# Kernel tuning notes

Hardware: AMD Instinct MI355X
Metric: run time of the kernel (lower is better)

The kernel has to match this reference:

```python
import jax, jax.numpy as jnp
from jax import lax
import numpy as np

B, C, H, W = 2, 64, 192, 192

def conv2d(x, w, pad):
    return lax.conv_general_dilated(x, w, (1, 1), [(pad, pad), (pad, pad)],
                                    dimension_numbers=('NCHW', 'OIHW', 'NCHW'))

def bilinear_sample(x, py, px):
    # x: [B,C,H,W]; py, px: [B,H,W] absolute fractional coords; zero padding outside.
    Bb, Cc, Hh, Ww = x.shape
    y0 = jnp.floor(py); x0 = jnp.floor(px)
    wy1 = py - y0; wx1 = px - x0
    xf = x.reshape(Bb, Cc, Hh * Ww)
    def gather(yi, xi):
        valid = (yi >= 0) & (yi < Hh) & (xi >= 0) & (xi < Ww)
        yc = jnp.clip(yi, 0, Hh - 1).astype(jnp.int32)
        xc = jnp.clip(xi, 0, Ww - 1).astype(jnp.int32)
        idx = (yc * Ww + xc).reshape(Bb, 1, Hh * Ww)
        v = jnp.take_along_axis(xf, idx, axis=2).reshape(Bb, Cc, Hh, Ww)
        return v * valid[:, None].astype(x.dtype)
    return (gather(y0, x0) * ((1 - wy1) * (1 - wx1))[:, None]
            + gather(y0, x0 + 1) * ((1 - wy1) * wx1)[:, None]
            + gather(y0 + 1, x0) * (wy1 * (1 - wx1))[:, None]
            + gather(y0 + 1, x0 + 1) * (wy1 * wx1)[:, None])

def deform_conv(x, w_off, b_off, w_mod, b_mod, w_reg, k):
    # torchvision deform_conv2d semantics with modulation (mask), stride=1, dilation=1.
    pad = k // 2
    offset = conv2d(x, w_off, pad) + b_off[None, :, None, None]   # [B,2*k*k,H,W] (y,x) interleaved
    mask = 2.0 * jax.nn.sigmoid(conv2d(x, w_mod, pad) + b_mod[None, :, None, None])  # [B,k*k,H,W]
    Bb, Cc, Hh, Ww = x.shape
    gy = jnp.arange(Hh, dtype=x.dtype)[None, :, None]
    gx = jnp.arange(Ww, dtype=x.dtype)[None, None, :]
    out = jnp.zeros((Bb, w_reg.shape[0], Hh, Ww), x.dtype)
    for i in range(k):          # fixed structural loop over kernel taps
        for j in range(k):
            t = i * k + j
            py = gy - pad + i + offset[:, 2 * t]
            px = gx - pad + j + offset[:, 2 * t + 1]
            samp = bilinear_sample(x, py, px) * mask[:, t][:, None]  # [B,C,H,W]
            out = out + jnp.einsum('bchw,oc->bohw', samp, w_reg[:, :, i, j])
    return out

def _branch(x, w_pre, w_off, b_off, w_mod, b_mod, w_reg, k):
    h = jax.nn.relu(conv2d(x, w_pre, 0))  # BasicConv 1x1 + ReLU (no bias)
    return deform_conv(h, w_off, b_off, w_mod, b_mod, w_reg, k)

def _forward(x_max, x_mid, x_small,
             w_pre_max, w_off_max, b_off_max, w_mod_max, b_mod_max, w_reg_max,
             w_pre_mid, w_off_mid, b_off_mid, w_mod_mid, b_mod_mid, w_reg_mid,
             w_pre_small, w_off_small, b_off_small, w_mod_small, b_mod_small, w_reg_small,
             w1, w2):
    y = x_max + x_mid + x_small
    a = _branch(x_max, w_pre_max, w_off_max, b_off_max, w_mod_max, b_mod_max, w_reg_max, 7)
    m = _branch(x_mid, w_pre_mid, w_off_mid, b_off_mid, w_mod_mid, b_mod_mid, w_reg_mid, 5)
    s = _branch(x_small, w_pre_small, w_off_small, b_off_small, w_mod_small, b_mod_small, w_reg_small, 3)
    x = jnp.tanh(m) * a
    x = jax.nn.relu(conv2d(x, w1, 0))
    x = jnp.tanh(s) * x
    x = jax.nn.relu(conv2d(x, w2, 0))
    return x + y

def setup_inputs() -> dict:
    key = jax.random.key(0)
    ks = jax.random.split(key, 32)
    d = {}
    d['x_max'] = jax.random.normal(ks[0], (B, C, H, W), jnp.float32)
    d['x_mid'] = jax.random.normal(ks[1], (B, C, H, W), jnp.float32)
    d['x_small'] = jax.random.normal(ks[2], (B, C, H, W), jnp.float32)
    i = 3
    for name, k in (('max', 7), ('mid', 5), ('small', 3)):
        d[f'w_pre_{name}'] = jax.random.normal(ks[i], (C, C, 1, 1), jnp.float32) * 0.05; i += 1
        d[f'w_off_{name}'] = jax.random.normal(ks[i], (2 * k * k, C, k, k), jnp.float32) * 0.01; i += 1
        d[f'b_off_{name}'] = jax.random.normal(ks[i], (2 * k * k,), jnp.float32) * 0.01; i += 1
        d[f'w_mod_{name}'] = jax.random.normal(ks[i], (k * k, C, k, k), jnp.float32) * 0.01; i += 1
        d[f'b_mod_{name}'] = jax.random.normal(ks[i], (k * k,), jnp.float32) * 0.01; i += 1
        d[f'w_reg_{name}'] = jax.random.normal(ks[i], (C, C, k, k), jnp.float32) * 0.02; i += 1
    d['w1'] = jax.random.normal(ks[i], (C, C, 1, 1), jnp.float32) * 0.05; i += 1
    d['w2'] = jax.random.normal(ks[i], (C, C, 1, 1), jnp.float32) * 0.05
    return d

def reference(x_max, x_mid, x_small,
              w_pre_max, w_off_max, b_off_max, w_mod_max, b_mod_max, w_reg_max,
              w_pre_mid, w_off_mid, b_off_mid, w_mod_mid, b_mod_mid, w_reg_mid,
              w_pre_small, w_off_small, b_off_small, w_mod_small, b_mod_small, w_reg_small,
              w1, w2):
    return _forward(x_max, x_mid, x_small,
                    w_pre_max, w_off_max, b_off_max, w_mod_max, b_mod_max, w_reg_max,
                    w_pre_mid, w_off_mid, b_off_mid, w_mod_mid, b_mod_mid, w_reg_mid,
                    w_pre_small, w_off_small, b_off_small, w_mod_small, b_mod_small, w_reg_small,
                    w1, w2)
```

## Files before the change

### kernel.cpp

```cpp
#include <hip/hip_runtime.h>
#include <hip/hip_bf16.h>
#include <math.h>

#define BB   2
#define CC   64
#define HH   192
#define WW   192
#define HW   (HH*WW)
#define HALO 3
#define HP   (HH + 2*HALO)
#define WP   (WW + 2*HALO)
#define PLANE (HP*WP)

typedef __attribute__((ext_vector_type(8))) _Float16 f16x8;
typedef __attribute__((ext_vector_type(4))) _Float16 f16x4;
typedef __attribute__((ext_vector_type(8))) unsigned short u16x8;
typedef __attribute__((ext_vector_type(4))) float f32x4;

__device__ __forceinline__ float fast_tanh(float x) {
    float e = __expf(2.f * x);
    return 1.f - 2.f * __builtin_amdgcn_rcpf(e + 1.f);
}
__device__ __forceinline__ f16x8 bc16(u16x8 v) { return __builtin_bit_cast(f16x8, v); }

__global__ __launch_bounds__(256) void conv_pre_k(
    const float* __restrict__ X0, const float* __restrict__ X1,
    const float* __restrict__ X2,
    const float* __restrict__ W0, const float* __restrict__ W1,
    const float* __restrict__ W2,
    u16x8* __restrict__ hp8all)
{
    __shared__ float wl[64*32];
    int tid = threadIdx.x;
    int oh  = blockIdx.y;
    int z   = blockIdx.z;
    const float* X = (z == 0) ? X0 : ((z == 1) ? X1 : X2);
    const float* W = (z == 0) ? W0 : ((z == 1) ? W1 : W2);
    u16x8* hp8 = hp8all + (size_t)z * ((size_t)BB*8*PLANE);

    #pragma unroll
    for (int n = 0; n < 8; n++) {
        int idx = tid + n*256;
        int op  = idx >> 6, c = idx & 63;
        wl[c*32 + op] = W[(size_t)(oh*32 + op)*64 + c];
    }
    __syncthreads();

    int p  = blockIdx.x*256 + tid;
    int b  = p / HW;
    int pp = p - b*HW;
    size_t base = (size_t)b*CC*HW + pp;

    float acc[32];
    #pragma unroll
    for (int o = 0; o < 32; o++) acc[o] = 0.f;

    #pragma unroll 4
    for (int c = 0; c < 64; c++) {
        float xv = X[base + (size_t)c*HW];
        const float4* w4 = (const float4*)(wl + c*32);
        #pragma unroll
        for (int q = 0; q < 8; q++) {
            float4 w = w4[q];
            acc[4*q+0] = fmaf(w.x, xv, acc[4*q+0]);
            acc[4*q+1] = fmaf(w.y, xv, acc[4*q+1]);
            acc[4*q+2] = fmaf(w.z, xv, acc[4*q+2]);
            acc[4*q+3] = fmaf(w.w, xv, acc[4*q+3]);
        }
    }

    int y = pp / WW, x = pp - y*WW;
    #pragma unroll
    for (int gq = 0; gq < 4; gq++) {
        u16x8 v;
        #pragma unroll
        for (int c = 0; c < 8; c++)
            v[c] = __builtin_bit_cast(unsigned short,
                     (_Float16)fmaxf(acc[gq*8+c], 0.f));
        hp8[(size_t)(b*8 + oh*4 + gq)*PLANE + (size_t)(y+HALO)*WP + (x+HALO)] = v;
    }
}

template<int MODE>
__global__ __launch_bounds__(256) void conv1x1_k(
    const _Float16* __restrict__ Xv, const _Float16* __restrict__ Mv,
    const float* __restrict__ W,
    const float* __restrict__ Y0, const float* __restrict__ Y1,
    const float* __restrict__ Y2,
    void* __restrict__ outv)
{
    __shared__ float wl[64*32];
    int tid = threadIdx.x;
    int oh  = blockIdx.y;
    #pragma unroll
    for (int n = 0; n < 8; n++) {
        int idx = tid + n*256;
        int op  = idx >> 6, c = idx & 63;
        wl[c*32 + op] = W[(size_t)(oh*32 + op)*64 + c];
    }
    __syncthreads();

    int p  = blockIdx.x*256 + tid;
    int b  = p / HW;
    int pp = p - b*HW;
    size_t base = (size_t)b*CC*HW + pp;

    float acc[32];
    #pragma unroll
    for (int o = 0; o < 32; o++) acc[o] = 0.f;

    #pragma unroll 4
    for (int c = 0; c < 64; c++) {
        float xv = (float)Xv[base + (size_t)c*HW];
        xv *= fast_tanh((float)Mv[base + (size_t)c*HW]);
        const float4* w4 = (const float4*)(wl + c*32);
        #pragma unroll
        for (int q = 0; q < 8; q++) {
            float4 w = w4[q];
            acc[4*q+0] = fmaf(w.x, xv, acc[4*q+0]);
            acc[4*q+1] = fmaf(w.y, xv, acc[4*q+1]);
            acc[4*q+2] = fmaf(w.z, xv, acc[4*q+2]);
            acc[4*q+3] = fmaf(w.w, xv, acc[4*q+3]);
        }
    }

    if (MODE == 1) {
        _Float16* op = (_Float16*)outv + base + (size_t)(oh*32)*HW;
        #pragma unroll
        for (int o = 0; o < 32; o++)
            op[(size_t)o*HW] = (_Float16)fmaxf(acc[o], 0.f);
    } else {
        float* op = (float*)outv + base + (size_t)(oh*32)*HW;
        size_t gi = base + (size_t)(oh*32)*HW;
        #pragma unroll
        for (int o = 0; o < 32; o++) {
            float yv = Y0[gi + (size_t)o*HW] + Y1[gi + (size_t)o*HW] + Y2[gi + (size_t)o*HW];
            op[(size_t)o*HW] = fmaxf(acc[o], 0.f) + yv;
        }
    }
}

template<int K>
__device__ void bake_wtb_dev(const float* __restrict__ Wreg,
                             f16x8* __restrict__ wtb, int t, int tid)
{
    constexpr int KK = K*K;
    for (int e = tid; e < 512; e += 256) {
        int kk = e >> 8, rem = e & 255;
        int ot = rem >> 6, l = rem & 63;
        int lr = l & 15, lg = l >> 4;
        int o  = ot*16 + lr;
        f16x8 v;
        #pragma unroll
        for (int j = 0; j < 8; j++) {
            int c = kk*32 + lg*8 + j;
            v[j] = (_Float16)Wreg[((size_t)o*CC + c)*KK + t];
        }
        wtb[(size_t)t*512 + e] = v;
    }
}
template<int K>
__device__ void bake_wbg_dev(const float* __restrict__ Woff,
                             const float* __restrict__ Wmod,
                             f16x8* __restrict__ wbg, int pos, int tid)
{
    constexpr int KK  = K*K;
    constexpr int NTF = (3*KK + 15)/16;
    for (int idx = tid; idx < 2*NTF*64; idx += 256) {
        int kk  = idx / (NTF*64);
        int rem = idx - kk*(NTF*64);
        int nt  = rem >> 6;
        int l   = rem & 63;
        int lg  = l >> 4, lr = l & 15;
        int n   = nt*16 + lr;
        f16x8 v;
        #pragma unroll
        for (int j = 0; j < 8; j++) {
            int c = kk*32 + lg*8 + j;
            float w = 0.f;
            if (n < 2*KK)      w = Woff[((size_t)n*CC + c)*KK + pos];
            else if (n < 3*KK) w = Wmod[((size_t)(n - 2*KK)*CC + c)*KK + pos];
            v[j] = (_Float16)w;
        }
        wbg[(size_t)pos*(2*NTF*64) + idx] = v;
    }
}
__global__ __launch_bounds__(256) void bake_all_k(
    const float* wreg7, const float* woff7, const float* wmod7,
    const float* wreg5, const float* woff5, const float* wmod5,
    const float* wreg3, const float* woff3, const float* wmod3,
    f16x8* wtb7, f16x8* wbg7, f16x8* wtb5, f16x8* wbg5,
    f16x8* wtb3, f16x8* wbg3)
{
    int blk = blockIdx.x, tid = threadIdx.x;
    if (blk < 49) {
        bake_wtb_dev<7>(wreg7, wtb7, blk, tid);
        bake_wbg_dev<7>(woff7, wmod7, wbg7, blk, tid);
    } else if (blk < 74) {
        int p = blk - 49;
        bake_wtb_dev<5>(wreg5, wtb5, p, tid);
        bake_wbg_dev<5>(woff5, wmod5, wbg5, p, tid);
    } else {
        int p = blk - 74;
        bake_wtb_dev<3>(wreg3, wtb3, p, tid);
        bake_wbg_dev<3>(woff3, wmod3, wbg3, p, tid);
    }
}

template<int K, int MT, int NS>
__global__ __launch_bounds__(256) void offmod_mfma_k(
    const u16x8* __restrict__ hp8,
    const f16x8* __restrict__ wbg,
    const float* __restrict__ Boff, const float* __restrict__ Bmod,
    _Float16* __restrict__ om)
{
    constexpr int PAD  = K/2;
    constexpr int KK   = K*K;
    constexpr int NTF  = (3*KK + 15)/16;
    constexpr int NT   = NTF/NS;
    constexpr int PBB  = HW/(64*MT);
    constexpr int NBLK = BB*PBB*NS;
    constexpr int PELEM = 2*NT*64;

    __shared__ f16x8 wl[2][PELEM];

    int raw = blockIdx.x;
    int swz = (raw & 7)*(NBLK >> 3) + (raw >> 3);
    int ng  = swz % NS;
    int s   = swz / NS;
    int b   = s / PBB;
    int blk = s - b*PBB;

    int tid  = threadIdx.x;
    int wave = tid >> 6;
    int l    = tid & 63;
    int lg   = l >> 4, lr = l & 15;
    int pxw  = blk*(4*MT*16) + wave*(MT*16);
    int y    = pxw / WW, x0 = pxw - y*WW;

    f32x4 acc[MT][NT];
    #pragma unroll
    for (int mt = 0; mt < MT; mt++)
        #pragma unroll
        for (int nt = 0; nt < NT; nt++) acc[mt][nt] = (f32x4)0.f;

    const u16x8* hb = hp8 + (size_t)(b*8)*PLANE;

    auto stage = [&](int buf, int pos) {
        #pragma unroll
        for (int ii = 0; ii < (PELEM + 255)/256; ii++) {
            int idx = tid + ii*256;
            if (PELEM % 256 == 0 || idx < PELEM) {
                int kk  = idx / (NT*64);
                int rem = idx - kk*(NT*64);
                int nt  = rem >> 6;
                int ll  = rem & 63;
                wl[buf][idx] = wbg[(size_t)pos*(2*NTF*64)
                                   + (size_t)(kk*NTF + ng*NT + nt)*64 + ll];
            }
        }
    };

    stage(0, 0);
    __syncthreads();

    int buf = 0;
    for (int pos = 0; pos < KK; pos++) {
        if (pos + 1 < KK) stage(buf ^ 1, pos + 1);

        int i = pos / K, j = pos - (pos/K)*K;
        int rbase = (y + HALO - PAD + i)*WP + (x0 + HALO - PAD + j);

        #pragma unroll
        for (int kk = 0; kk < 2; kk++) {
            const f16x8* G = (const f16x8*)(hb + (size_t)(kk*4 + lg)*PLANE + rbase);
            f16x8 a[MT];
            #pragma unroll
            for (int mt = 0; mt < MT; mt++) a[mt] = G[mt*16 + lr];
            #pragma unroll
            for (int nt = 0; nt < NT; nt++) {
                f16x8 bf = wl[buf][(kk*NT + nt)*64 + l];
                #pragma unroll
                for (int mt = 0; mt < MT; mt++)
                    acc[mt][nt] = __builtin_amdgcn_mfma_f32_16x16x32_f16(
                        a[mt], bf, acc[mt][nt], 0, 0, 0);
            }
        }
        __syncthreads();
        buf ^= 1;
    }

    #pragma unroll
    for (int nt = 0; nt < NT; nt++) {
        int n = ng*NT*16 + nt*16 + lr;
        if (n < 3*KK) {
            bool is_mask = (n >= 2*KK);
            float bias = is_mask ? Bmod[n - 2*KK] : Boff[n];
            _Float16* dst0 = om + ((size_t)b*3*KK + n)*HW + pxw + lg*4;
            #pragma unroll
            for (int mt = 0; mt < MT; mt++) {
                f32x4 v = acc[mt][nt];
                float v0 = v[0] + bias, v1 = v[1] + bias, v2 = v[2] + bias, v3 = v[3] + bias;
                if (is_mask) {
                    v0 = 2.f * __builtin_amdgcn_rcpf(1.f + __expf(-v0));
                    v1 = 2.f * __builtin_amdgcn_rcpf(1.f + __expf(-v1));
                    v2 = 2.f * __builtin_amdgcn_rcpf(1.f + __expf(-v2));
                    v3 = 2.f * __builtin_amdgcn_rcpf(1.f + __expf(-v3));
                }
                f16x4 o;
                o[0] = (_Float16)v0; o[1] = (_Float16)v1;
                o[2] = (_Float16)v2; o[3] = (_Float16)v3;
                *reinterpret_cast<f16x4*>(dst0 + mt*16) = o;
            }
        }
    }
}

template<int K>
__global__ __launch_bounds__(256, 4) void deform_mfma_k(
    const u16x8* __restrict__ hp8,
    const _Float16* __restrict__ om,
    const f16x8* __restrict__ wtb,
    _Float16* __restrict__ out)
{
    constexpr int PAD = K/2;
    constexpr int KK  = K*K;
    constexpr int NSB = HW/16;
    constexpr int HWW = K + 2;
    constexpr int WWW = 16 + K + 2;
    constexpr int WELEMS = 8*HWW*WWW;
    constexpr int NPT = KK*16;
    constexpr int COORD_B = NPT*8 + NPT*4 + ((NPT*2 + 15)/16)*16;
    constexpr int RED_B   = 2*64*16*4;
    constexpr int UNION_B = (COORD_B > RED_B ? COORD_B : RED_B);

    __shared__ u16x8 win[8][HWW][WWW];
    __shared__ __align__(16) char ubuf[UNION_B];

    f16x4*          hco  = (f16x4*)ubuf;
    unsigned*       gofs = (unsigned*)(ubuf + NPT*8);
    unsigned short* wofs = (unsigned short*)(ubuf + NPT*8 + NPT*4);

    int raw = blockIdx.x;
    int swz = (raw & 7)*((BB*NSB) >> 3) + (raw >> 3);
    int b = swz / NSB, strip = swz - b*NSB;

    int tid  = threadIdx.x;
    int wave = tid >> 6;
    int l    = tid & 63;
    int lg   = l >> 4;
    int lr   = l & 15;
    int th   = wave & 1;
    int kkh  = wave >> 1;
    int pxbase = strip*16;
    int y    = pxbase / WW;
    int xs   = pxbase - y*WW;

    int wy0 = y  + HALO - PAD - 1;
    int wx0 = xs + HALO - PAD - 1;

    {
        const u16x8* hbb = hp8 + (size_t)(b*8)*PLANE;
        for (int idx = tid; idx < WELEMS; idx += 256) {
            int g  = idx / (HWW*WWW);
            int r2 = idx - g*(HWW*WWW);
            int r  = r2 / WWW;
            int c2 = r2 - r*WWW;
            int gy = min(max(wy0 + r, 0), HP-1);
            int gx = min(max(wx0 + c2, 0), WP-1);
            win[g][r][c2] = hbb[(size_t)g*PLANE + gy*WP + gx];
        }
    }
    {
        const _Float16* ob = om + (size_t)b*3*KK*HW + pxbase;
        for (int idx = tid; idx < NPT; idx += 256) {
            int pxl = idx & 15, t = idx >> 4;
            float offy = (float)ob[(size_t)(2*t  )*HW + pxl];
            float offx = (float)ob[(size_t)(2*t+1)*HW + pxl];
            float mk   = (float)ob[(size_t)(2*KK+t)*HW + pxl];
            int i = t / K, j = t - (t/K)*K;
            float py  = (float)(y - PAD + i) + offy;
            float pxf = (float)(xs + pxl - PAD + j) + offx;
            float fy = floorf(py), fx = floorf(pxf);
            float wy1 = py - fy, wx1 = pxf - fx;
            int iy0 = (int)fy, ix0 = (int)fx;
            int Y0 = min(max(iy0, -1), HH) + HALO;
            int X0 = min(max(ix0, -1), WW) + HALO;
            int ry = Y0 - wy0, rx = X0 - wx0;
            bool in = ((unsigned)ry <= (unsigned)(HWW-2)) &
                      ((unsigned)rx <= (unsigned)(WWW-2));
            f16x4 h;
            h[0] = (_Float16)((1.f-wy1)*(1.f-wx1)*mk);
            h[1] = (_Float16)((1.f-wy1)*wx1*mk);
            h[2] = (_Float16)(wy1*(1.f-wx1)*mk);
            h[3] = (_Float16)(wy1*wx1*mk);
            hco[idx]  = h;
            gofs[idx] = (unsigned)(Y0*WP + X0);
            wofs[idx] = (unsigned short)((ry*WWW + rx) | (in ? 0 : 0x8000));
        }
    }
    __syncthreads();

    int t0 = (KK*th)/2, t1 = (KK*(th+1))/2;

    f32x4 acc[4];
    #pragma unroll
    for (int ot = 0; ot < 4; ot++) acc[ot] = (f32x4)0.f;

    const u16x8* hb   = hp8 + (size_t)(b*8 + kkh*4 + lg)*PLANE;
    const u16x8* wing = &win[kkh*4 + lg][0][0];

    #pragma unroll 1
    for (int t = t0; t < t1; t++) {
        int idx = t*16 + lr;
        f16x4 h = hco[idx];
        unsigned short wf = wofs[idx];
        bool in = (wf & 0x8000) == 0;

        f16x8 c0, c1, c2, c3;
        if (__all(in)) {
            const u16x8* Wp = wing + wf;
            c0 = bc16(Wp[0]);   c1 = bc16(Wp[1]);
            c2 = bc16(Wp[WWW]); c3 = bc16(Wp[WWW+1]);
        } else {
            const u16x8* G = hb + gofs[idx];
            c0 = bc16(G[0]);  c1 = bc16(G[1]);
            c2 = bc16(G[WP]); c3 = bc16(G[WP+1]);
        }

        f16x8 s = c0*h[0] + c1*h[1] + c2*h[2] + c3*h[3];

        const f16x8* bp = wtb + (size_t)t*8*64 + l;
        #pragma unroll
        for (int ot = 0; ot < 4; ot++) {
            acc[ot] = __builtin_amdgcn_mfma_f32_16x16x32_f16(
                s, bp[(size_t)(kkh*4 + ot)*64], acc[ot], 0, 0, 0);
        }
    }

    __syncthreads();
    float* redf = (float*)ubuf;
    #define RIDX(tt, o, g)  (((tt)*64 + (o))*16 + (((g) ^ ((o) & 3)) * 4))
    if (kkh == 1) {
        #pragma unroll
        for (int ot = 0; ot < 4; ot++) {
            int o = ot*16 + lr;
            *reinterpret_cast<f32x4*>(&redf[RIDX(th, o, lg)]) = acc[ot];
        }
    }
    __syncthreads();
    if (kkh == 0) {
        #pragma unroll
        for (int ot = 0; ot < 4; ot++) {
            int o = ot*16 + lr;
            acc[ot] += *reinterpret_cast<const f32x4*>(&redf[RIDX(th, o, lg)]);
        }
    }
    __syncthreads();
    if (kkh == 0 && th == 1) {
        #pragma unroll
        for (int ot = 0; ot < 4; ot++) {
            int o = ot*16 + lr;
            *reinterpret_cast<f32x4*>(&redf[RIDX(0, o, lg)]) = acc[ot];
        }
    }
    __syncthreads();
    if (kkh == 0 && th == 0) {
        _Float16* ob = out + (size_t)b*CC*HW + pxbase + lg*4;
        #pragma unroll
        for (int ot = 0; ot < 4; ot++) {
            int o = ot*16 + lr;
            f32x4 rr = *reinterpret_cast<const f32x4*>(&redf[RIDX(0, o, lg)]);
            rr += acc[ot];
            f16x4 v;
            v[0] = (_Float16)rr[0]; v[1] = (_Float16)rr[1];
            v[2] = (_Float16)rr[2]; v[3] = (_Float16)rr[3];
            *reinterpret_cast<f16x4*>(ob + (size_t)o*HW) = v;
        }
    }
    #undef RIDX
}

extern "C" void kernel_launch(void* const* d_in, const int* in_sizes, int n_in,
                              void* d_out, int out_size, void* d_ws, size_t ws_size,
                              hipStream_t stream)
{
    const float* x_max      = (const float*)d_in[0];
    const float* x_mid      = (const float*)d_in[1];
    const float* x_small    = (const float*)d_in[2];
    const float* w_pre_max  = (const float*)d_in[3];
    const float* w_off_max  = (const float*)d_in[4];
    const float* b_off_max  = (const float*)d_in[5];
    const float* w_mod_max  = (const float*)d_in[6];
    const float* b_mod_max  = (const float*)d_in[7];
    const float* w_reg_max  = (const float*)d_in[8];
    const float* w_pre_mid  = (const float*)d_in[9];
    const float* w_off_mid  = (const float*)d_in[10];
    const float* b_off_mid  = (const float*)d_in[11];
    const float* w_mod_mid  = (const float*)d_in[12];
    const float* b_mod_mid  = (const float*)d_in[13];
    const float* w_reg_mid  = (const float*)d_in[14];
    const float* w_pre_small= (const float*)d_in[15];
    const float* w_off_small= (const float*)d_in[16];
    const float* b_off_small= (const float*)d_in[17];
    const float* w_mod_small= (const float*)d_in[18];
    const float* b_mod_small= (const float*)d_in[19];
    const float* w_reg_small= (const float*)d_in[20];
    const float* w1         = (const float*)d_in[21];
    const float* w2         = (const float*)d_in[22];

    float* out = (float*)d_out;
    char*  ws  = (char*)d_ws;

    const size_t HPB = (size_t)BB*8*PLANE;

    u16x8*    hp8 = (u16x8*)ws;                 ws += 3*HPB*16;
    _Float16* om  = (_Float16*)ws;              ws += (size_t)BB*3*49*HW*2;
    _Float16* aa  = (_Float16*)ws;              ws += (size_t)BB*CC*HW*2;
    _Float16* mm  = (_Float16*)ws;              ws += (size_t)BB*CC*HW*2;
    _Float16* sm  = (_Float16*)ws;              ws += (size_t)BB*CC*HW*2;
    _Float16* u   = (_Float16*)ws;              ws += (size_t)BB*CC*HW*2;
    f16x8*    wtb7= (f16x8*)ws;                 ws += (size_t)49*512*16;
    f16x8*    wbg7= (f16x8*)ws;                 ws += (size_t)49*2*10*64*16;
    f16x8*    wtb5= (f16x8*)ws;                 ws += (size_t)25*512*16;
    f16x8*    wbg5= (f16x8*)ws;                 ws += (size_t)25*2*5*64*16;
    f16x8*    wtb3= (f16x8*)ws;                 ws += (size_t)9*512*16;
    f16x8*    wbg3= (f16x8*)ws;

    hipMemsetAsync(hp8, 0, 3*HPB*16, stream);

    const int npix_blocks = (BB*HW)/256;
    const int dfm_blocks  = BB*(HW/16);
    const int off7_blocks = BB*(HW/128)*5;
    const int off5_blocks = BB*(HW/128)*5;
    const int off3_blocks = BB*(HW/128)*2;

    bake_all_k<<<83, 256, 0, stream>>>(
        w_reg_max, w_off_max, w_mod_max,
        w_reg_mid, w_off_mid, w_mod_mid,
        w_reg_small, w_off_small, w_mod_small,
        wtb7, wbg7, wtb5, wbg5, wtb3, wbg3);
    conv_pre_k<<<dim3(npix_blocks, 2, 3), 256, 0, stream>>>(
        x_max, x_mid, x_small, w_pre_max, w_pre_mid, w_pre_small, hp8);

    offmod_mfma_k<7,2,5><<<off7_blocks, 256, 0, stream>>>(
        hp8 + 0*HPB, wbg7, b_off_max, b_mod_max, om);
    deform_mfma_k<7><<<dfm_blocks, 256, 0, stream>>>(hp8 + 0*HPB, om, wtb7, aa);

    offmod_mfma_k<5,2,5><<<off5_blocks, 256, 0, stream>>>(
        hp8 + 1*HPB, wbg5, b_off_mid, b_mod_mid, om);
    deform_mfma_k<5><<<dfm_blocks, 256, 0, stream>>>(hp8 + 1*HPB, om, wtb5, mm);

    offmod_mfma_k<3,2,2><<<off3_blocks, 256, 0, stream>>>(
        hp8 + 2*HPB, wbg3, b_off_small, b_mod_small, om);
    deform_mfma_k<3><<<dfm_blocks, 256, 0, stream>>>(hp8 + 2*HPB, om, wtb3, sm);

    conv1x1_k<1><<<dim3(npix_blocks,2), 256, 0, stream>>>(aa, mm, w1,
                                                  nullptr, nullptr, nullptr, u);
    conv1x1_k<2><<<dim3(npix_blocks,2), 256, 0, stream>>>(u, sm, w2,
                                                  x_max, x_mid, x_small, out);
}
```

Measured before the change: 449.0 us.

## Drop LDS weight staging in offset/mask conv and retune tile splits

The offset/mask MFMA conv now loads its B-fragment weights straight from global memory (through cache) instead of double-buffering them in shared memory, which removes the per-tap __syncthreads barriers. The per-branch output-channel split (NS) and pixel tile (MT) are retuned, so each block computes more output channels and the grid is smaller. A launch-bounds occupancy hint is also added. In exchange, every wave issues redundant global weight loads, and the larger per-thread accumulator count may raise register pressure.

New measurement: 476.8 us. 6.2% more time.

```diff
diff --git a/kernel.cpp b/kernel.cpp
--- a/kernel.cpp
+++ b/kernel.cpp
@@ -208,7 +208,7 @@
 }
 
 template<int K, int MT, int NS>
-__global__ __launch_bounds__(256) void offmod_mfma_k(
+__global__ __launch_bounds__(256, 6) void offmod_mfma_k(
     const u16x8* __restrict__ hp8,
     const f16x8* __restrict__ wbg,
     const float* __restrict__ Boff, const float* __restrict__ Bmod,
@@ -220,9 +220,6 @@
     constexpr int NT   = NTF/NS;
     constexpr int PBB  = HW/(64*MT);
     constexpr int NBLK = BB*PBB*NS;
-    constexpr int PELEM = 2*NT*64;
-
-    __shared__ f16x8 wl[2][PELEM];
 
     int raw = blockIdx.x;
     int swz = (raw & 7)*(NBLK >> 3) + (raw >> 3);
@@ -245,31 +242,13 @@
         for (int nt = 0; nt < NT; nt++) acc[mt][nt] = (f32x4)0.f;
 
     const u16x8* hb = hp8 + (size_t)(b*8)*PLANE;
-
-    auto stage = [&](int buf, int pos) {
-        #pragma unroll
-        for (int ii = 0; ii < (PELEM + 255)/256; ii++) {
-            int idx = tid + ii*256;
-            if (PELEM % 256 == 0 || idx < PELEM) {
-                int kk  = idx / (NT*64);
-                int rem = idx - kk*(NT*64);
-                int nt  = rem >> 6;
-                int ll  = rem & 63;
-                wl[buf][idx] = wbg[(size_t)pos*(2*NTF*64)
-                                   + (size_t)(kk*NTF + ng*NT + nt)*64 + ll];
-            }
-        }
-    };
-
-    stage(0, 0);
-    __syncthreads();
-
-    int buf = 0;
+    const f16x8* wb = wbg + l;
+
+    #pragma unroll 1
     for (int pos = 0; pos < KK; pos++) {
-        if (pos + 1 < KK) stage(buf ^ 1, pos + 1);
-
         int i = pos / K, j = pos - (pos/K)*K;
         int rbase = (y + HALO - PAD + i)*WP + (x0 + HALO - PAD + j);
+        const f16x8* wp = wb + (size_t)pos*(2*NTF*64);
 
         #pragma unroll
         for (int kk = 0; kk < 2; kk++) {
@@ -279,15 +258,13 @@
             for (int mt = 0; mt < MT; mt++) a[mt] = G[mt*16 + lr];
             #pragma unroll
             for (int nt = 0; nt < NT; nt++) {
-                f16x8 bf = wl[buf][(kk*NT + nt)*64 + l];
+                f16x8 bf = wp[(size_t)(kk*NTF + ng*NT + nt)*64];
                 #pragma unroll
                 for (int mt = 0; mt < MT; mt++)
                     acc[mt][nt] = __builtin_amdgcn_mfma_f32_16x16x32_f16(
                         a[mt], bf, acc[mt][nt], 0, 0, 0);
             }
         }
-        __syncthreads();
-        buf ^= 1;
     }
 
     #pragma unroll
@@ -531,9 +508,9 @@
 
     const int npix_blocks = (BB*HW)/256;
     const int dfm_blocks  = BB*(HW/16);
-    const int off7_blocks = BB*(HW/128)*5;
-    const int off5_blocks = BB*(HW/128)*5;
-    const int off3_blocks = BB*(HW/128)*2;
+    const int off7_blocks = BB*(HW/128)*2;
+    const int off5_blocks = BB*(HW/64);
+    const int off3_blocks = BB*(HW/128);
 
     bake_all_k<<<83, 256, 0, stream>>>(
         w_reg_max, w_off_max, w_mod_max,
@@ -543,15 +520,15 @@
     conv_pre_k<<<dim3(npix_blocks, 2, 3), 256, 0, stream>>>(
         x_max, x_mid, x_small, w_pre_max, w_pre_mid, w_pre_small, hp8);
 
-    offmod_mfma_k<7,2,5><<<off7_blocks, 256, 0, stream>>>(
+    offmod_mfma_k<7,2,2><<<off7_blocks, 256, 0, stream>>>(
         hp8 + 0*HPB, wbg7, b_off_max, b_mod_max, om);
     deform_mfma_k<7><<<dfm_blocks, 256, 0, stream>>>(hp8 + 0*HPB, om, wtb7, aa);
 
-    offmod_mfma_k<5,2,5><<<off5_blocks, 256, 0, stream>>>(
+    offmod_mfma_k<5,1,1><<<off5_blocks, 256, 0, stream>>>(
         hp8 + 1*HPB, wbg5, b_off_mid, b_mod_mid, om);
     deform_mfma_k<5><<<dfm_blocks, 256, 0, stream>>>(hp8 + 1*HPB, om, wtb5, mm);
 
-    offmod_mfma_k<3,2,2><<<off3_blocks, 256, 0, stream>>>(
+    offmod_mfma_k<3,2,1><<<off3_blocks, 256, 0, stream>>>(
         hp8 + 2*HPB, wbg3, b_off_small, b_mod_small, om);
     deform_mfma_k<3><<<dfm_blocks, 256, 0, stream>>>(hp8 + 2*HPB, om, wtb3, sm);
 
```
